# Optimization experiments

Measured on AMD Instinct MI355X. Metric: run time of the kernel, lower is better.

Reference implementation:

```python
import jax, jax.numpy as jnp
import numpy as np

N_OBJS = 15
C_OUT = 2
KP_THRES = 0.95
IOU_THRES = 0.45
N_R, N_SHP, N_EXP = 9, 199, 29
PDIM = N_R + N_SHP + N_EXP
RESIZE = 320
NUM_ANCHORS = 2
SENTINEL = -1e30  # marks non-detected candidate boxes so they never match NMS output


def _anchor_centers(stride):
    hw = RESIZE // stride
    X, Y = jnp.meshgrid(jnp.arange(hw), jnp.arange(hw))
    ac = (jnp.stack([X, Y], -1) * stride).reshape(-1, 2)
    # stack([c]*2, axis=1).reshape(-1,2) == interleaved repeat
    return jnp.repeat(ac, NUM_ANCHORS, axis=0).astype(jnp.float32)  # (A,2)


def _process_level(cls, bbox, param, stride, pms, u_base, shp_base, exp_base, r):
    B, A, _ = cls.shape
    prob = jax.nn.sigmoid(cls)                      # (B,A,2)
    mask = prob > KP_THRES
    ac = _anchor_centers(stride)                    # (A,2)
    d = bbox * stride
    x1 = ac[:, 0] - d[..., 0]; y1 = ac[:, 1] - d[..., 1]
    x2 = ac[:, 0] + d[..., 2]; y2 = ac[:, 1] + d[..., 3]
    boxes = jnp.stack([x1, y1, x2, y2], -1).reshape(B, A, 2, 2)   # rows [x1,y1],[x2,y2]
    # 3DMM param decode
    p = param * pms[1] + pms[0]
    R = p[..., :N_R].reshape(B, A, 3, 3)
    shp = p[..., N_R:N_R + N_SHP]
    exp = p[..., N_R + N_SHP:]
    ln = u_base[:, 0] + shp @ shp_base.T + exp @ exp_base.T       # (B,A,204)
    ln = jnp.einsum('bakd,bacd->bakc', ln.reshape(B, A, 68, 3), R)[..., :2]  # lnmks @ R^T, keep xy
    tl = ln.min(-2, keepdims=True); br = ln.max(-2, keepdims=True)
    scale = (boxes[:, :, 1:, :] - boxes[:, :, :1, :]) / (br - tl)
    ln = jnp.abs(scale) * ln                         # (B,A,68,2)
    boxes_yx = boxes[..., ::-1] * r                  # (x,y)->(y,x), scale to original image
    ln_yx = ln[..., ::-1] * r
    boxes5 = jnp.concatenate(
        [jnp.broadcast_to(boxes_yx.reshape(B, A, 1, 4), (B, A, C_OUT, 4)), prob[..., None]], -1)
    ln_c = jnp.broadcast_to(ln_yx[:, :, None], (B, A, C_OUT, 68, 2))
    bidx = jnp.broadcast_to(jnp.arange(B)[:, None, None], (B, A, C_OUT)).reshape(-1)
    cidx = jnp.broadcast_to(jnp.arange(C_OUT)[None, None, :], (B, A, C_OUT)).reshape(-1)
    return mask.reshape(-1), boxes5.reshape(-1, 5), ln_c.reshape(-1, 68, 2), bidx, cidx


def _greedy_nms(boxes, scores, k, iou_thres):
    # NMS selection indices are constants w.r.t. AD (like tf.image NMS)
    boxes = jax.lax.stop_gradient(boxes)
    scores = jax.lax.stop_gradient(scores)
    n = scores.shape[0]
    area = jnp.clip(boxes[:, 2] - boxes[:, 0], 0) * jnp.clip(boxes[:, 3] - boxes[:, 1], 0)

    def step(carry, i):
        active, sel = carry
        s = jnp.where(active, scores, -jnp.inf)
        j = jnp.argmax(s)
        valid = s[j] > -jnp.inf
        sel = sel.at[i].set(jnp.where(valid, j.astype(jnp.int32), -1))
        tl = jnp.maximum(boxes[j, :2], boxes[:, :2])
        br = jnp.minimum(boxes[j, 2:], boxes[:, 2:])
        inter = jnp.prod(jnp.clip(br - tl, 0), -1)
        union = area[j] + area - inter
        iou = jnp.where(union > 0, inter / union, 0.0)
        active = active & (iou <= iou_thres)
        active = active.at[j].set(False)
        active = active & valid
        return (active, sel), None

    (_, sel), _ = jax.lax.scan(step, (jnp.ones(n, bool), -jnp.ones(k, jnp.int32)), jnp.arange(k))
    return sel


def _combined_nms(boxes, scores):
    # boxes (n_objs, C_OUT, 4) [y1,x1,y2,x2] per class, scores (n_objs, C_OUT)
    bs, ss, cs = [], [], []
    for c in range(C_OUT):
        sel = _greedy_nms(boxes[:, c], scores[:, c], N_OBJS, IOU_THRES)
        valid = sel >= 0
        si = jnp.clip(sel, 0)
        bs.append(boxes[si, c])
        ss.append(jnp.where(valid, scores[si, c], -jnp.inf))
        cs.append(jnp.full((N_OBJS,), float(c), jnp.float32))
    b = jnp.concatenate(bs); s = jnp.concatenate(ss); cl = jnp.concatenate(cs)
    order = jnp.argsort(-s)[:N_OBJS]
    b, s, cl = b[order], s[order], cl[order]
    valid = s > -jnp.inf
    return (jnp.where(valid[:, None], b, 0.0), jnp.where(valid, s, 0.0), jnp.where(valid, cl, 0.0))


def _forward(cls_16, bbox_16, param_16, cls_32, bbox_32, param_32,
             origin_shapes, pms, u_base, shp_base, exp_base):
    r = (origin_shapes / float(RESIZE))[0]            # (2,) -> einsum over b with b==1
    B = cls_16.shape[0]
    out_boxes = -jnp.ones((B, N_OBJS, C_OUT, 5), jnp.float32)
    cand_boxes, cand_ln, cand_idx = [], [], []
    levels = ((cls_16, bbox_16, param_16, 16), (cls_32, bbox_32, param_32, 32))  # stride 8 skipped
    for cls, bbox, param, stride in levels:
        mask, boxes5, ln, bidx, cidx = _process_level(
            cls, bbox, param, stride, pms, u_base, shp_base, exp_base, r)
        oidx = jnp.cumsum(mask) - 1                   # tf.where row-major detection order
        oidx = jnp.where(mask, oidx, N_OBJS).astype(jnp.int32)  # OOB -> dropped (TF-GPU scatter semantics)
        out_boxes = out_boxes.at[bidx, oidx, cidx].set(boxes5, mode='drop')
        cand_boxes.append(jnp.where(mask[:, None], boxes5[:, :4], SENTINEL))
        cand_ln.append(ln)
        cand_idx.append(jnp.stack([bidx, oidx, cidx], -1))
    bbox_tensor = jnp.concatenate(cand_boxes)         # (N,4)
    lnmk_tensor = jnp.concatenate(cand_ln)            # (N,68,2)
    idxs_tensor = jnp.concatenate(cand_idx)           # (N,3)

    scores = out_boxes[..., -1]                       # (B,n,2)
    boxes_pc = out_boxes[..., :-1]                    # (B,n,2,4)
    nms_b, nms_s, nms_c = jax.vmap(_combined_nms)(boxes_pc, scores)

    box_results = jnp.where(nms_b == -1.0, jnp.inf, nms_b)    # (B,n,4)
    flat = box_results.reshape(-1, 4)
    match = jnp.all(flat[:, None, :] == bbox_tensor[None, :, :], -1)  # (B*n, N)
    matched = match.any(-1)
    cand = jnp.argmax(match, -1)
    ln_sel = lnmk_tensor[cand]
    idx_sel = jnp.where(matched[:, None], idxs_tensor[cand], jnp.array([0, N_OBJS, 0], jnp.int32))
    out_ln = -jnp.ones((B, N_OBJS, C_OUT, 68, 2), jnp.float32)
    out_ln = out_ln.at[idx_sel[:, 0], idx_sel[:, 1], idx_sel[:, 2]].set(ln_sel, mode='drop')
    out_ln = jnp.where(out_ln == -1.0, jnp.inf, out_ln)

    box_results = jnp.where(box_results - 1.0 == -1.0, jnp.inf, box_results)
    bb = jnp.concatenate([box_results, nms_s[..., None], nms_c[..., None]], -1)
    bb = jnp.where(bb == -1.0, jnp.inf, bb)
    return bb.reshape(-1, N_OBJS, 6), out_ln


def setup_inputs() -> dict:
    key = jax.random.key(0)
    ks = jax.random.split(key, 14)
    B = 32
    rn = lambda k, shp, s=1.0: jax.random.normal(k, shp, jnp.float32) * s
    return {
        'cls_8': rn(ks[0], (B, 3200, 2)),
        'bbox_8': jax.random.uniform(ks[1], (B, 3200, 4), jnp.float32),
        'param_8': rn(ks[2], (B, 3200, PDIM)),
        'cls_16': rn(ks[3], (B, 800, 2)),
        'bbox_16': jax.random.uniform(ks[4], (B, 800, 4), jnp.float32),
        'param_16': rn(ks[5], (B, 800, PDIM)),
        'cls_32': rn(ks[6], (B, 200, 2)),
        'bbox_32': jax.random.uniform(ks[7], (B, 200, 4), jnp.float32),
        'param_32': rn(ks[8], (B, 200, PDIM)),
        'origin_shapes': jnp.ones((1, 2), jnp.float32) * 640.0,
        'pms': jnp.concatenate([rn(ks[9], (1, PDIM), 0.05),
                                jax.random.uniform(ks[10], (1, PDIM), jnp.float32) * 0.05], 0),
        'u_base': rn(ks[11], (204, 1)),
        'shp_base': rn(ks[12], (204, 199), 0.01),
        'exp_base': rn(ks[13], (204, 29), 0.01),
    }


def reference(cls_8, bbox_8, param_8, cls_16, bbox_16, param_16,
              cls_32, bbox_32, param_32, origin_shapes, pms, u_base, shp_base, exp_base):
    # level-0 (stride 8) feats are accepted but skipped, matching the original `continue`
    return _forward(cls_16, bbox_16, param_16, cls_32, bbox_32, param_32,
                    origin_shapes, pms, u_base, shp_base, exp_base)
```

## Files before the change

kernel.cpp:

```cpp
#include <hip/hip_runtime.h>
#include <math.h>


#define BIGF  3.0e38f

#define B_    32
#define A16   800
#define A32   200
#define NOBJ  15
#define NCLS  2
#define CAP   512
#define SMAX  256
#define N16FLAT (B_*A16*NCLS)
#define NFLAT   (N16FLAT + B_*A32*NCLS)
#define PDIM  237
#define NR    9
#define NSHP  199
#define NEXP  29
#define KTOT  (NSHP + NEXP)
#define NROW  204
#define NCHUNK 4
#define CHK   (KTOT/NCHUNK)
#define CHKF  (CHK*NROW)
#define CHKF4 (CHKF/4)

#define OFF_CNT    0
#define OFF_N      1
#define OFF_N16    2
#define OFF_GLIST  16
#define OFF_SORTG  (OFF_GLIST + CAP)
#define OFF_OIDX   (OFF_SORTG + CAP)
#define OFF_CBOX   (OFF_OIDX + CAP)
#define OFF_CSCORE (OFF_CBOX + 4*CAP)
#define OFF_OUTB   (OFF_CSCORE + CAP)
#define OFF_BR1    (OFF_OUTB + B_*NOBJ*NCLS*5)
#define OFF_CLN    (OFF_BR1 + B_*NOBJ*4)
#define OFF_BT     (OFF_CLN + CAP*136)

#define OUT_LN_OFF (B_*NOBJ*6)
#define LN_SIZE    (B_*NOBJ*NCLS*68*2)
#define LN_SIZE4   (LN_SIZE/4)
#define OUTB_SZ4   (B_*NOBJ*NCLS*5/4)
#define INIT4      (LN_SIZE4 + OUTB_SZ4)
#define BT_N       (KTOT*NROW)
#define IM_THREADS 46592

__device__ __forceinline__ void decode_g(int g, int& lvl, int& b, int& a, int& c) {
  if (g < N16FLAT) {
    lvl = 0; b = g / (A16*NCLS); int q = g % (A16*NCLS); a = q >> 1; c = q & 1;
  } else {
    int g2 = g - N16FLAT;
    lvl = 1; b = g2 / (A32*NCLS); int q = g2 % (A32*NCLS); a = q >> 1; c = q & 1;
  }
}

__device__ __forceinline__ float sigm(float x) { return 1.0f / (1.0f + expf(-x)); }

__device__ __forceinline__ float pick15(const float (&a)[NOBJ], int j) {
  float r = a[0];
  #pragma unroll
  for (int i = 1; i < NOBJ; ++i) r = (j == i) ? a[i] : r;
  return r;
}

__global__ void k_initmask(const float* __restrict__ cls16,
                           const float* __restrict__ cls32,
                           const float* __restrict__ shpb,
                           const float* __restrict__ expb,
                           float* __restrict__ out, float* __restrict__ ws) {
  int t = blockIdx.x * blockDim.x + threadIdx.x;
  if (t < LN_SIZE4)
    ((float4*)(out + OUT_LN_OFF))[t] = make_float4(BIGF, BIGF, BIGF, BIGF);
  else if (t < INIT4)
    ((float4*)(ws + OFF_OUTB))[t - LN_SIZE4] = make_float4(-1.f, -1.f, -1.f, -1.f);
  const int N16F4 = N16FLAT/4, NF4 = NFLAT/4;
  if (t < NF4) {
    float4 v; int base;
    if (t < N16F4) { v = ((const float4*)cls16)[t]; base = 4*t; }
    else { v = ((const float4*)cls32)[t - N16F4]; base = N16FLAT + 4*(t - N16F4); }
    float vv[4] = {v.x, v.y, v.z, v.w};
    #pragma unroll
    for (int k = 0; k < 4; ++k) {
      if (sigm(vv[k]) > 0.95f) {
        int pos = atomicAdd(&((int*)ws)[OFF_CNT], 1);
        if (pos < CAP) ((int*)ws)[OFF_GLIST + pos] = base + k;
      }
    }
  }
  if (t < BT_N) {
    int row = t % NROW, k = t / NROW;
    float v = (k < NSHP) ? shpb[(size_t)row*NSHP + k]
                         : expb[(size_t)row*NEXP + (k - NSHP)];
    ws[OFF_BT + t] = v;
  }
}

__global__ void k_prep(const float* __restrict__ cls16, const float* __restrict__ bbox16,
                       const float* __restrict__ cls32, const float* __restrict__ bbox32,
                       const float* __restrict__ oshapes, float* __restrict__ ws) {
  __shared__ int s_gl[CAP];
  __shared__ int s_sorted[CAP];
  __shared__ int sh_n16;
  int tid = threadIdx.x;
  int* wi = (int*)ws;
  int n = wi[OFF_CNT]; if (n > CAP) n = CAP;
  if (tid == 0) { wi[OFF_N] = n; sh_n16 = 0; }
  for (int i = tid; i < n; i += blockDim.x) s_gl[i] = wi[OFF_GLIST + i];
  __syncthreads();

  int loc16 = 0;
  for (int i = tid; i < n; i += blockDim.x) {
    int gi = s_gl[i];
    int rank = 0;
    for (int j = 0; j < n; ++j) rank += (s_gl[j] < gi);
    s_sorted[rank] = gi;
    loc16 += (gi < N16FLAT);
  }
  if (loc16) atomicAdd(&sh_n16, loc16);
  __syncthreads();
  int n16 = sh_n16;
  if (tid == 0) wi[OFF_N16] = n16;

  float r0 = oshapes[0] / 320.0f;
  float r1 = oshapes[1] / 320.0f;

  for (int s = tid; s < n; s += blockDim.x) {
    int g = s_sorted[s];
    wi[OFF_SORTG + s] = g;
    int lvl, b, a, c; decode_g(g, lvl, b, a, c);
    int oidx = (s < n16) ? s : (s - n16);
    wi[OFF_OIDX + s] = oidx;
    const float* cls = lvl ? cls32 : cls16;
    const float* bbp = lvl ? bbox32 : bbox16;
    int A = lvl ? A32 : A16;
    int hw = lvl ? 10 : 20;
    float stride = lvl ? 32.f : 16.f;
    float prob = sigm(cls[(b*A + a)*2 + c]);
    int pos = a >> 1;
    float acx = (float)(pos % hw) * stride;
    float acy = (float)(pos / hw) * stride;
    const float* bp = bbp + (size_t)(b*A + a) * 4;
    float x1 = acx - bp[0]*stride, y1 = acy - bp[1]*stride;
    float x2 = acx + bp[2]*stride, y2 = acy + bp[3]*stride;
    ws[OFF_CBOX + 4*s + 0] = y1 * r0;
    ws[OFF_CBOX + 4*s + 1] = x1 * r1;
    ws[OFF_CBOX + 4*s + 2] = y2 * r0;
    ws[OFF_CBOX + 4*s + 3] = x2 * r1;
    ws[OFF_CSCORE + s] = prob;
  }
  __syncthreads();
  int lim16 = (n16 < NOBJ) ? n16 : NOBJ;
  for (int s = tid; s < lim16; s += blockDim.x) {
    int g = s_sorted[s]; int lvl, b, a, c; decode_g(g, lvl, b, a, c);
    int base = ((b*NOBJ + s)*NCLS + c) * 5;
    for (int k = 0; k < 4; ++k) ws[OFF_OUTB + base + k] = ws[OFF_CBOX + 4*s + k];
    ws[OFF_OUTB + base + 4] = ws[OFF_CSCORE + s];
  }
  __syncthreads();
  int lim32 = ((n - n16) < NOBJ) ? (n - n16) : NOBJ;
  for (int t2 = tid; t2 < lim32; t2 += blockDim.x) {
    int s = n16 + t2;
    int g = s_sorted[s]; int lvl, b, a, c; decode_g(g, lvl, b, a, c);
    int base = ((b*NOBJ + t2)*NCLS + c) * 5;
    for (int k = 0; k < 4; ++k) ws[OFF_OUTB + base + k] = ws[OFF_CBOX + 4*s + k];
    ws[OFF_OUTB + base + 4] = ws[OFF_CSCORE + s];
  }
}

union SharedU {
  struct {
    float4 bt4[CHKF4];
    float p[PDIM];
    float l204[NROW];
    float l2[136];
    float sc01[2];
  } land;
  struct {
    float s_outb[B_*NOBJ*NCLS*5];
    int   lsel[B_*NCLS*NOBJ];
  } nms;
};

__global__ void __launch_bounds__(256)
k_landnms(const float* __restrict__ param16,
          const float* __restrict__ param32,
          const float* __restrict__ bbox16,
          const float* __restrict__ bbox32,
          const float* __restrict__ pms,
          const float* __restrict__ ubase,
          const float* __restrict__ oshapes,
          float* __restrict__ ws, float* __restrict__ out) {
  __shared__ SharedU su;
  int tid = threadIdx.x;
  int bid = blockIdx.x;
  int* wi = (int*)ws;

  if (bid < SMAX) {
    int n = wi[OFF_N]; if (n > SMAX) n = SMAX;
    int s = bid;
    if (s >= n) return;
    int g = wi[OFF_SORTG + s];
    int lvl, b, a, c; decode_g(g, lvl, b, a, c);
    int A = lvl ? A32 : A16;
    const float* par = (lvl ? param32 : param16) + (size_t)(b*A + a) * PDIM;
    if (tid < PDIM) su.land.p[tid] = fmaf(par[tid], pms[PDIM + tid], pms[tid]);
    __syncthreads();
    float acc = 0.f;
    for (int ch = 0; ch < NCHUNK; ++ch) {
      const float4* src = (const float4*)(ws + OFF_BT + ch*CHKF);
      for (int i = tid; i < CHKF4; i += 256) su.land.bt4[i] = src[i];
      __syncthreads();
      if (tid < NROW) {
        const float* sb = (const float*)su.land.bt4;
        #pragma unroll 19
        for (int kk = 0; kk < CHK; ++kk)
          acc = fmaf(su.land.p[NR + ch*CHK + kk], sb[kk*NROW + tid], acc);
      }
      __syncthreads();
    }
    if (tid < NROW) su.land.l204[tid] = ubase[tid] + acc;
    __syncthreads();
    if (tid < 68) {
      float v0 = su.land.l204[3*tid], v1 = su.land.l204[3*tid+1], v2 = su.land.l204[3*tid+2];
      su.land.l2[2*tid]     = v0*su.land.p[0] + v1*su.land.p[1] + v2*su.land.p[2];
      su.land.l2[2*tid + 1] = v0*su.land.p[3] + v1*su.land.p[4] + v2*su.land.p[5];
    }
    __syncthreads();
    if (tid < 64) {
      int lane = tid;
      float mn0 = INFINITY, mx0 = -INFINITY, mn1 = INFINITY, mx1 = -INFINITY;
      for (int k = lane; k < 68; k += 64) {
        float x = su.land.l2[2*k], y = su.land.l2[2*k+1];
        mn0 = fminf(mn0, x); mx0 = fmaxf(mx0, x);
        mn1 = fminf(mn1, y); mx1 = fmaxf(mx1, y);
      }
      #pragma unroll
      for (int off = 32; off > 0; off >>= 1) {
        mn0 = fminf(mn0, __shfl_down(mn0, off)); mx0 = fmaxf(mx0, __shfl_down(mx0, off));
        mn1 = fminf(mn1, __shfl_down(mn1, off)); mx1 = fmaxf(mx1, __shfl_down(mx1, off));
      }
      if (lane == 0) {
        float stride = lvl ? 32.f : 16.f;
        int hw = lvl ? 10 : 20;
        int pos = a >> 1;
        float acx = (float)(pos % hw) * stride;
        float acy = (float)(pos / hw) * stride;
        const float* bp = (lvl ? bbox32 : bbox16) + (size_t)(b*A + a) * 4;
        float x1 = acx - bp[0]*stride, x2 = acx + bp[2]*stride;
        float y1 = acy - bp[1]*stride, y2 = acy + bp[3]*stride;
        su.land.sc01[0] = fabsf((x2 - x1) / (mx0 - mn0));
        su.land.sc01[1] = fabsf((y2 - y1) / (mx1 - mn1));
      }
    }
    __syncthreads();
    if (tid < 68) {
      float r0 = oshapes[0] / 320.0f, r1 = oshapes[1] / 320.0f;
      float lx = su.land.sc01[0] * su.land.l2[2*tid];
      float ly = su.land.sc01[1] * su.land.l2[2*tid + 1];
      ws[OFF_CLN + (size_t)s*136 + 2*tid]     = ly * r0;
      ws[OFF_CLN + (size_t)s*136 + 2*tid + 1] = lx * r1;
    }
  } else {
    for (int i = tid; i < B_*NOBJ*NCLS*5; i += blockDim.x)
      su.nms.s_outb[i] = ws[OFF_OUTB + i];
    __syncthreads();
    if (tid < B_*NCLS) {
      int b = tid >> 1, c = tid & 1;
      float bx0[NOBJ], bx1[NOBJ], bx2[NOBJ], bx3[NOBJ], sc[NOBJ], ar[NOBJ];
      #pragma unroll
      for (int i = 0; i < NOBJ; ++i) {
        int base = ((b*NOBJ + i)*NCLS + c) * 5;
        bx0[i] = su.nms.s_outb[base+0];
        bx1[i] = su.nms.s_outb[base+1];
        bx2[i] = su.nms.s_outb[base+2];
        bx3[i] = su.nms.s_outb[base+3];
        sc[i]  = su.nms.s_outb[base+4];
        float dy = bx2[i] - bx0[i]; if (dy < 0.f) dy = 0.f;
        float dx = bx3[i] - bx1[i]; if (dx < 0.f) dx = 0.f;
        ar[i] = dy * dx;
      }
      unsigned act = (1u << NOBJ) - 1;
      for (int it = 0; it < NOBJ; ++it) {
        float best = -INFINITY; int j = -1;
        #pragma unroll
        for (int i = 0; i < NOBJ; ++i)
          if ((act >> i) & 1) { if (sc[i] > best) { best = sc[i]; j = i; } }
        if (j < 0) { su.nms.lsel[tid*NOBJ + it] = -1; act = 0; continue; }
        su.nms.lsel[tid*NOBJ + it] = j;
        float j0 = pick15(bx0, j), j1 = pick15(bx1, j);
        float j2 = pick15(bx2, j), j3 = pick15(bx3, j);
        float aj = pick15(ar, j);
        #pragma unroll
        for (int i = 0; i < NOBJ; ++i) {
          float tly = fmaxf(j0, bx0[i]);
          float tlx = fmaxf(j1, bx1[i]);
          float bry = fminf(j2, bx2[i]);
          float brx = fminf(j3, bx3[i]);
          float iy = bry - tly; if (iy < 0.f) iy = 0.f;
          float ix = brx - tlx; if (ix < 0.f) ix = 0.f;
          float inter = iy * ix;
          float uni = aj + ar[i] - inter;
          float iou = (uni > 0.f) ? (inter / uni) : 0.f;
          if (!(iou <= 0.45f)) act &= ~(1u << i);
        }
        act &= ~(1u << j);
      }
    }
    __syncthreads();
    if (tid < B_) {
      int b = tid;
      float es[2*NOBJ];
      #pragma unroll
      for (int e = 0; e < 2*NOBJ; ++e) {
        int c = (e >= NOBJ), i = e - c*NOBJ;
        int sl = su.nms.lsel[(b*NCLS + c)*NOBJ + i];
        int si = (sl >= 0) ? sl : 0;
        es[e] = (sl >= 0) ? su.nms.s_outb[((b*NOBJ + si)*NCLS + c)*5 + 4]
                          : -INFINITY;
      }
      unsigned used = 0;
      for (int r = 0; r < NOBJ; ++r) {
        int j = -1; float best = 0.f;
        #pragma unroll
        for (int e = 0; e < 2*NOBJ; ++e) {
          if ((used >> e) & 1) continue;
          float v = es[e];
          if (j < 0 || v > best) { j = e; best = v; }
        }
        used |= 1u << j;
        float sv = best;
        bool valid = sv > -INFINITY;
        int c = (j >= NOBJ), i = j - c*NOBJ;
        int sl = su.nms.lsel[(b*NCLS + c)*NOBJ + i];
        int si = (sl >= 0) ? sl : 0;
        int base = ((b*NOBJ + si)*NCLS + c) * 5;
        float ns  = valid ? sv : 0.f;
        float ncl = valid ? (float)c : 0.f;
        for (int k = 0; k < 4; ++k) {
          float nb = valid ? su.nms.s_outb[base + k] : 0.f;
          float b1 = (nb == -1.0f) ? BIGF : nb;
          ws[OFF_BR1 + (b*NOBJ + r)*4 + k] = b1;
          float b2 = ((b1 - 1.0f) == -1.0f) ? BIGF : b1;
          float b3 = (b2 == -1.0f) ? BIGF : b2;
          out[(b*NOBJ + r)*6 + k] = b3;
        }
        out[(b*NOBJ + r)*6 + 4] = (ns  == -1.0f) ? BIGF : ns;
        out[(b*NOBJ + r)*6 + 5] = (ncl == -1.0f) ? BIGF : ncl;
      }
    }
  }
}

__global__ void k_match(float* __restrict__ ws, float* __restrict__ out) {
  __shared__ float s_cbox[4*CAP];
  int* wi = (int*)ws;
  int n = wi[OFF_N];
  for (int i = threadIdx.x; i < 4*n; i += blockDim.x) s_cbox[i] = ws[OFF_CBOX + i];
  __syncthreads();
  int t = blockIdx.x * blockDim.x + threadIdx.x;
  if (t >= B_*NOBJ) return;
  float q0 = ws[OFF_BR1 + 4*t + 0], q1 = ws[OFF_BR1 + 4*t + 1];
  float q2 = ws[OFF_BR1 + 4*t + 2], q3 = ws[OFF_BR1 + 4*t + 3];
  int ms = -1;
  for (int s = 0; s < n; ++s) {
    if (s_cbox[4*s] == q0 && s_cbox[4*s+1] == q1 &&
        s_cbox[4*s+2] == q2 && s_cbox[4*s+3] == q3) { ms = s; break; }
  }
  if (ms < 0) return;
  int oidx = wi[OFF_OIDX + ms];
  if (oidx >= NOBJ) return;
  int g = wi[OFF_SORTG + ms];
  int lvl, b, a, c; decode_g(g, lvl, b, a, c);
  float4* dst = (float4*)(out + OUT_LN_OFF + (size_t)((b*NOBJ + oidx)*NCLS + c) * 136);
  const float4* src = (const float4*)(ws + OFF_CLN + (size_t)ms * 136);
  for (int k = 0; k < 34; ++k) dst[k] = src[k];
}

extern "C" void kernel_launch(void* const* d_in, const int* in_sizes, int n_in,
                              void* d_out, int out_size, void* d_ws, size_t ws_size,
                              hipStream_t stream) {
  const float* cls16   = (const float*)d_in[3];
  const float* bbox16  = (const float*)d_in[4];
  const float* param16 = (const float*)d_in[5];
  const float* cls32   = (const float*)d_in[6];
  const float* bbox32  = (const float*)d_in[7];
  const float* param32 = (const float*)d_in[8];
  const float* oshapes = (const float*)d_in[9];
  const float* pms     = (const float*)d_in[10];
  const float* ubase   = (const float*)d_in[11];
  const float* shpb    = (const float*)d_in[12];
  const float* expb    = (const float*)d_in[13];
  float* out = (float*)d_out;
  float* ws  = (float*)d_ws;

  hipMemsetAsync(ws, 0, 64, stream);
  k_initmask<<<(IM_THREADS + 255)/256, 256, 0, stream>>>(cls16, cls32, shpb, expb, out, ws);
  k_prep<<<1, 256, 0, stream>>>(cls16, bbox16, cls32, bbox32, oshapes, ws);
  k_landnms<<<SMAX + 1, 256, 0, stream>>>(param16, param32, bbox16, bbox32,
                                          pms, ubase, oshapes, ws, out);
  k_match<<<2, 256, 0, stream>>>(ws, out);
}
```

Baseline: 228.9 us.

## Parallelize per-batch NMS across blocks and wavefronts with shuffle argmax

Per-class greedy NMS and the cross-class top-k merge used to run in one block, with one thread per (batch, class) working through serial register loops. Now each batch gets its own block, each class gets a wavefront with one lane per candidate, and argmax selection uses a shuffle-xor reduction. This shortens the serial tail of the fused landmark/NMS kernel at the cost of 31 more blocks and per-iteration wave reductions. Tie-breaking by lowest index is meant to keep the original selection order.

Result: faster. 203.8 us (-11.0%).

```diff
diff --git a/kernel.cpp b/kernel.cpp
--- a/kernel.cpp
+++ b/kernel.cpp
@@ -45,6 +45,8 @@
 #define BT_N       (KTOT*NROW)
 #define IM_THREADS 46592
 
+#define NMS_BLOCKS B_
+
 __device__ __forceinline__ void decode_g(int g, int& lvl, int& b, int& a, int& c) {
   if (g < N16FLAT) {
     lvl = 0; b = g / (A16*NCLS); int q = g % (A16*NCLS); a = q >> 1; c = q & 1;
@@ -56,11 +58,13 @@
 
 __device__ __forceinline__ float sigm(float x) { return 1.0f / (1.0f + expf(-x)); }
 
-__device__ __forceinline__ float pick15(const float (&a)[NOBJ], int j) {
-  float r = a[0];
+__device__ __forceinline__ void wave_argmax(float& v, int& idx) {
   #pragma unroll
-  for (int i = 1; i < NOBJ; ++i) r = (j == i) ? a[i] : r;
-  return r;
+  for (int off = 1; off < 64; off <<= 1) {
+    float ov = __shfl_xor(v, off);
+    int   oi = __shfl_xor(idx, off);
+    if (ov > v || (ov == v && oi < idx)) { v = ov; idx = oi; }
+  }
 }
 
 __global__ void k_initmask(const float* __restrict__ cls16,
@@ -167,18 +171,12 @@
   }
 }
 
-union SharedU {
-  struct {
-    float4 bt4[CHKF4];
-    float p[PDIM];
-    float l204[NROW];
-    float l2[136];
-    float sc01[2];
-  } land;
-  struct {
-    float s_outb[B_*NOBJ*NCLS*5];
-    int   lsel[B_*NCLS*NOBJ];
-  } nms;
+struct SharedLand {
+  float4 bt4[CHKF4];
+  float p[PDIM];
+  float l204[NROW];
+  float l2[136];
+  float sc01[2];
 };
 
 __global__ void __launch_bounds__(256)
@@ -190,7 +188,9 @@
           const float* __restrict__ ubase,
           const float* __restrict__ oshapes,
           float* __restrict__ ws, float* __restrict__ out) {
-  __shared__ SharedU su;
+  __shared__ SharedLand su;
+  __shared__ int   s_lsel[NCLS*NOBJ];
+  __shared__ float s_lsc[NCLS*NOBJ];
   int tid = threadIdx.x;
   int bid = blockIdx.x;
   int* wi = (int*)ws;
@@ -203,34 +203,34 @@
     int lvl, b, a, c; decode_g(g, lvl, b, a, c);
     int A = lvl ? A32 : A16;
     const float* par = (lvl ? param32 : param16) + (size_t)(b*A + a) * PDIM;
-    if (tid < PDIM) su.land.p[tid] = fmaf(par[tid], pms[PDIM + tid], pms[tid]);
+    if (tid < PDIM) su.p[tid] = fmaf(par[tid], pms[PDIM + tid], pms[tid]);
     __syncthreads();
     float acc = 0.f;
     for (int ch = 0; ch < NCHUNK; ++ch) {
       const float4* src = (const float4*)(ws + OFF_BT + ch*CHKF);
-      for (int i = tid; i < CHKF4; i += 256) su.land.bt4[i] = src[i];
+      for (int i = tid; i < CHKF4; i += 256) su.bt4[i] = src[i];
       __syncthreads();
       if (tid < NROW) {
-        const float* sb = (const float*)su.land.bt4;
+        const float* sb = (const float*)su.bt4;
         #pragma unroll 19
         for (int kk = 0; kk < CHK; ++kk)
-          acc = fmaf(su.land.p[NR + ch*CHK + kk], sb[kk*NROW + tid], acc);
+          acc = fmaf(su.p[NR + ch*CHK + kk], sb[kk*NROW + tid], acc);
       }
       __syncthreads();
     }
-    if (tid < NROW) su.land.l204[tid] = ubase[tid] + acc;
+    if (tid < NROW) su.l204[tid] = ubase[tid] + acc;
     __syncthreads();
     if (tid < 68) {
-      float v0 = su.land.l204[3*tid], v1 = su.land.l204[3*tid+1], v2 = su.land.l204[3*tid+2];
-      su.land.l2[2*tid]     = v0*su.land.p[0] + v1*su.land.p[1] + v2*su.land.p[2];
-      su.land.l2[2*tid + 1] = v0*su.land.p[3] + v1*su.land.p[4] + v2*su.land.p[5];
+      float v0 = su.l204[3*tid], v1 = su.l204[3*tid+1], v2 = su.l204[3*tid+2];
+      su.l2[2*tid]     = v0*su.p[0] + v1*su.p[1] + v2*su.p[2];
+      su.l2[2*tid + 1] = v0*su.p[3] + v1*su.p[4] + v2*su.p[5];
     }
     __syncthreads();
     if (tid < 64) {
       int lane = tid;
       float mn0 = INFINITY, mx0 = -INFINITY, mn1 = INFINITY, mx1 = -INFINITY;
       for (int k = lane; k < 68; k += 64) {
-        float x = su.land.l2[2*k], y = su.land.l2[2*k+1];
+        float x = su.l2[2*k], y = su.l2[2*k+1];
         mn0 = fminf(mn0, x); mx0 = fmaxf(mx0, x);
         mn1 = fminf(mn1, y); mx1 = fmaxf(mx1, y);
       }
@@ -248,104 +248,102 @@
         const float* bp = (lvl ? bbox32 : bbox16) + (size_t)(b*A + a) * 4;
         float x1 = acx - bp[0]*stride, x2 = acx + bp[2]*stride;
         float y1 = acy - bp[1]*stride, y2 = acy + bp[3]*stride;
-        su.land.sc01[0] = fabsf((x2 - x1) / (mx0 - mn0));
-        su.land.sc01[1] = fabsf((y2 - y1) / (mx1 - mn1));
+        su.sc01[0] = fabsf((x2 - x1) / (mx0 - mn0));
+        su.sc01[1] = fabsf((y2 - y1) / (mx1 - mn1));
       }
     }
     __syncthreads();
     if (tid < 68) {
       float r0 = oshapes[0] / 320.0f, r1 = oshapes[1] / 320.0f;
-      float lx = su.land.sc01[0] * su.land.l2[2*tid];
-      float ly = su.land.sc01[1] * su.land.l2[2*tid + 1];
+      float lx = su.sc01[0] * su.l2[2*tid];
+      float ly = su.sc01[1] * su.l2[2*tid + 1];
       ws[OFF_CLN + (size_t)s*136 + 2*tid]     = ly * r0;
       ws[OFF_CLN + (size_t)s*136 + 2*tid + 1] = lx * r1;
     }
   } else {
-    for (int i = tid; i < B_*NOBJ*NCLS*5; i += blockDim.x)
-      su.nms.s_outb[i] = ws[OFF_OUTB + i];
+    int b = bid - SMAX;
+    int w = tid >> 6, lane = tid & 63;
+    if (w < NCLS) {
+      int c = w;
+      float b0 = 0.f, b1 = 0.f, b2 = 0.f, b3 = 0.f, sc = -INFINITY, ar = 0.f;
+      if (lane < NOBJ) {
+        int base = ((b*NOBJ + lane)*NCLS + c) * 5;
+        b0 = ws[OFF_OUTB + base + 0];
+        b1 = ws[OFF_OUTB + base + 1];
+        b2 = ws[OFF_OUTB + base + 2];
+        b3 = ws[OFF_OUTB + base + 3];
+        sc = ws[OFF_OUTB + base + 4];
+        float dy = b2 - b0; if (dy < 0.f) dy = 0.f;
+        float dx = b3 - b1; if (dx < 0.f) dx = 0.f;
+        ar = dy * dx;
+      }
+      bool alive = (lane < NOBJ);
+      for (int it = 0; it < NOBJ; ++it) {
+        float v = alive ? sc : -INFINITY;
+        int idx = lane;
+        wave_argmax(v, idx);
+        bool valid = v > -INFINITY;
+        if (lane == 0) {
+          s_lsel[c*NOBJ + it] = valid ? idx : -1;
+          s_lsc [c*NOBJ + it] = valid ? v : -INFINITY;
+        }
+        float j0 = __shfl(b0, idx), j1 = __shfl(b1, idx);
+        float j2 = __shfl(b2, idx), j3 = __shfl(b3, idx);
+        float ja = __shfl(ar, idx);
+        float tly = fmaxf(j0, b0);
+        float tlx = fmaxf(j1, b1);
+        float bry = fminf(j2, b2);
+        float brx = fminf(j3, b3);
+        float iy = bry - tly; if (iy < 0.f) iy = 0.f;
+        float ix = brx - tlx; if (ix < 0.f) ix = 0.f;
+        float inter = iy * ix;
+        float uni = ja + ar - inter;
+        float iou = (uni > 0.f) ? (inter / uni) : 0.f;
+        alive = alive && (iou <= 0.45f) && (lane != idx) && valid;
+      }
+    }
     __syncthreads();
-    if (tid < B_*NCLS) {
-      int b = tid >> 1, c = tid & 1;
-      float bx0[NOBJ], bx1[NOBJ], bx2[NOBJ], bx3[NOBJ], sc[NOBJ], ar[NOBJ];
-      #pragma unroll
-      for (int i = 0; i < NOBJ; ++i) {
-        int base = ((b*NOBJ + i)*NCLS + c) * 5;
-        bx0[i] = su.nms.s_outb[base+0];
-        bx1[i] = su.nms.s_outb[base+1];
-        bx2[i] = su.nms.s_outb[base+2];
-        bx3[i] = su.nms.s_outb[base+3];
-        sc[i]  = su.nms.s_outb[base+4];
-        float dy = bx2[i] - bx0[i]; if (dy < 0.f) dy = 0.f;
-        float dx = bx3[i] - bx1[i]; if (dx < 0.f) dx = 0.f;
-        ar[i] = dy * dx;
-      }
-      unsigned act = (1u << NOBJ) - 1;
-      for (int it = 0; it < NOBJ; ++it) {
-        float best = -INFINITY; int j = -1;
-        #pragma unroll
-        for (int i = 0; i < NOBJ; ++i)
-          if ((act >> i) & 1) { if (sc[i] > best) { best = sc[i]; j = i; } }
-        if (j < 0) { su.nms.lsel[tid*NOBJ + it] = -1; act = 0; continue; }
-        su.nms.lsel[tid*NOBJ + it] = j;
-        float j0 = pick15(bx0, j), j1 = pick15(bx1, j);
-        float j2 = pick15(bx2, j), j3 = pick15(bx3, j);
-        float aj = pick15(ar, j);
-        #pragma unroll
-        for (int i = 0; i < NOBJ; ++i) {
-          float tly = fmaxf(j0, bx0[i]);
-          float tlx = fmaxf(j1, bx1[i]);
-          float bry = fminf(j2, bx2[i]);
-          float brx = fminf(j3, bx3[i]);
-          float iy = bry - tly; if (iy < 0.f) iy = 0.f;
-          float ix = brx - tlx; if (ix < 0.f) ix = 0.f;
-          float inter = iy * ix;
-          float uni = aj + ar[i] - inter;
-          float iou = (uni > 0.f) ? (inter / uni) : 0.f;
-          if (!(iou <= 0.45f)) act &= ~(1u << i);
-        }
-        act &= ~(1u << j);
-      }
-    }
-    __syncthreads();
-    if (tid < B_) {
-      int b = tid;
-      float es[2*NOBJ];
-      #pragma unroll
-      for (int e = 0; e < 2*NOBJ; ++e) {
-        int c = (e >= NOBJ), i = e - c*NOBJ;
-        int sl = su.nms.lsel[(b*NCLS + c)*NOBJ + i];
-        int si = (sl >= 0) ? sl : 0;
-        es[e] = (sl >= 0) ? su.nms.s_outb[((b*NOBJ + si)*NCLS + c)*5 + 4]
-                          : -INFINITY;
-      }
-      unsigned used = 0;
-      for (int r = 0; r < NOBJ; ++r) {
-        int j = -1; float best = 0.f;
-        #pragma unroll
-        for (int e = 0; e < 2*NOBJ; ++e) {
-          if ((used >> e) & 1) continue;
-          float v = es[e];
-          if (j < 0 || v > best) { j = e; best = v; }
-        }
-        used |= 1u << j;
-        float sv = best;
-        bool valid = sv > -INFINITY;
-        int c = (j >= NOBJ), i = j - c*NOBJ;
-        int sl = su.nms.lsel[(b*NCLS + c)*NOBJ + i];
+    if (w == 0) {
+      float sv = -INFINITY;
+      float bx0 = 0.f, bx1 = 0.f, bx2 = 0.f, bx3 = 0.f;
+      int c = 0;
+      bool used = (lane >= NCLS*NOBJ);
+      if (lane < NCLS*NOBJ) {
+        c = lane / NOBJ;
+        int sl = s_lsel[lane];
+        sv = s_lsc[lane];
         int si = (sl >= 0) ? sl : 0;
         int base = ((b*NOBJ + si)*NCLS + c) * 5;
-        float ns  = valid ? sv : 0.f;
-        float ncl = valid ? (float)c : 0.f;
-        for (int k = 0; k < 4; ++k) {
-          float nb = valid ? su.nms.s_outb[base + k] : 0.f;
-          float b1 = (nb == -1.0f) ? BIGF : nb;
-          ws[OFF_BR1 + (b*NOBJ + r)*4 + k] = b1;
-          float b2 = ((b1 - 1.0f) == -1.0f) ? BIGF : b1;
-          float b3 = (b2 == -1.0f) ? BIGF : b2;
-          out[(b*NOBJ + r)*6 + k] = b3;
+        bx0 = ws[OFF_OUTB + base + 0];
+        bx1 = ws[OFF_OUTB + base + 1];
+        bx2 = ws[OFF_OUTB + base + 2];
+        bx3 = ws[OFF_OUTB + base + 3];
+      }
+      for (int r = 0; r < NOBJ; ++r) {
+        float v = used ? -INFINITY : sv;
+        int idx = lane;
+        wave_argmax(v, idx);
+        if (lane == idx) {
+          used = true;
+          bool valid = sv > -INFINITY;
+          float ns  = valid ? sv : 0.f;
+          float ncl = valid ? (float)c : 0.f;
+          float nb[4];
+          nb[0] = valid ? bx0 : 0.f;
+          nb[1] = valid ? bx1 : 0.f;
+          nb[2] = valid ? bx2 : 0.f;
+          nb[3] = valid ? bx3 : 0.f;
+          #pragma unroll
+          for (int k = 0; k < 4; ++k) {
+            float b1v = (nb[k] == -1.0f) ? BIGF : nb[k];
+            ws[OFF_BR1 + (b*NOBJ + r)*4 + k] = b1v;
+            float b2v = ((b1v - 1.0f) == -1.0f) ? BIGF : b1v;
+            float b3v = (b2v == -1.0f) ? BIGF : b2v;
+            out[(b*NOBJ + r)*6 + k] = b3v;
+          }
+          out[(b*NOBJ + r)*6 + 4] = (ns  == -1.0f) ? BIGF : ns;
+          out[(b*NOBJ + r)*6 + 5] = (ncl == -1.0f) ? BIGF : ncl;
         }
-        out[(b*NOBJ + r)*6 + 4] = (ns  == -1.0f) ? BIGF : ns;
-        out[(b*NOBJ + r)*6 + 5] = (ncl == -1.0f) ? BIGF : ncl;
       }
     }
   }
@@ -396,7 +394,7 @@
   hipMemsetAsync(ws, 0, 64, stream);
   k_initmask<<<(IM_THREADS + 255)/256, 256, 0, stream>>>(cls16, cls32, shpb, expb, out, ws);
   k_prep<<<1, 256, 0, stream>>>(cls16, bbox16, cls32, bbox32, oshapes, ws);
-  k_landnms<<<SMAX + 1, 256, 0, stream>>>(param16, param32, bbox16, bbox32,
-                                          pms, ubase, oshapes, ws, out);
+  k_landnms<<<SMAX + NMS_BLOCKS, 256, 0, stream>>>(param16, param32, bbox16, bbox32,
+                                                   pms, ubase, oshapes, ws, out);
   k_match<<<2, 256, 0, stream>>>(ws, out);
 }
```
